# Optimization experiments

Measured on AMD Instinct MI355X. Metric: run time of the kernel, lower is better.

## Reference

```python
import jax, jax.numpy as jnp
import numpy as np

N = 100000          # nodes
C = 25000           # clusters in coding tree
E = 1000000         # edges
D = 64              # num_features == hidden_dim
NUM_BLOCKS = 2
N_CONVS = 2 * NUM_BLOCKS + 1
BN_EPS = 1e-5


def setup_inputs() -> dict:
    key = jax.random.key(0)
    ks = jax.random.split(key, 8)
    sc = 1.0 / np.sqrt(D)
    x = jax.random.normal(ks[0], (N, D), jnp.float32)
    edge_index = jax.random.randint(ks[1], (2, E), 0, N, dtype=jnp.int32)
    s_cluster = jax.random.randint(ks[2], (N,), 0, C, dtype=jnp.int32)
    conv_w = jax.random.normal(ks[3], (N_CONVS, D, D), jnp.float32) * sc
    conv_b = jnp.zeros((N_CONVS, D), jnp.float32)
    pool_w = jax.random.normal(ks[4], (2, D, D), jnp.float32) * sc
    pool_b = jnp.zeros((2, D), jnp.float32)
    bn_gamma = jnp.ones((2, D), jnp.float32)
    bn_beta = jnp.zeros((2, D), jnp.float32)
    return {"x": x, "edge_index": edge_index, "s_cluster": s_cluster,
            "conv_w": conv_w, "conv_b": conv_b, "pool_w": pool_w,
            "pool_b": pool_b, "bn_gamma": bn_gamma, "bn_beta": bn_beta}


def _gcn_norm(edge_index):
    # GCNConv default: add self-loops, symmetric normalization D^-1/2 (A+I) D^-1/2
    loop = jnp.arange(N, dtype=edge_index.dtype)
    row = jnp.concatenate([edge_index[0], loop])  # source nodes
    col = jnp.concatenate([edge_index[1], loop])  # target nodes
    deg = jax.ops.segment_sum(jnp.ones(row.shape[0], jnp.float32), col, num_segments=N)
    dinv = jnp.where(deg > 0, jax.lax.rsqrt(deg), 0.0)
    return row, col, dinv[row] * dinv[col]  # per-edge norm coefficient


def _gcn_conv(x, w, b, row, col, norm):
    h = x @ w                                     # [N, D] transform first (PyG GCNConv)
    msg = h[row] * norm[:, None]                  # gather + scale, [E+N, D]
    return jax.ops.segment_sum(msg, col, num_segments=N) + b


def _sepool(x, src_idx, dst_idx, out_size, w, b, gamma, beta):
    # SEPooling: scatter-add aggregation then nn = Linear -> ReLU -> BatchNorm1d
    agg = jax.ops.segment_sum(x[src_idx], dst_idx, num_segments=out_size)
    h = jax.nn.relu(agg @ w + b)
    mean = jnp.mean(h, axis=0)
    var = jnp.mean((h - mean) ** 2, axis=0)       # biased var, torch BN training mode
    return gamma * (h - mean) * jax.lax.rsqrt(var + BN_EPS) + beta


def reference(x, edge_index, s_cluster, conv_w, conv_b, pool_w, pool_b, bn_gamma, bn_beta):
    row, col, norm = _gcn_norm(edge_index)
    node_ids = jnp.arange(N, dtype=s_cluster.dtype)
    for i in range(NUM_BLOCKS):
        x = jax.nn.relu(_gcn_conv(x, conv_w[i], conv_b[i], row, col, norm))
    # pool down: nodes -> clusters (s_edge_index = [cluster, node], target_to_source)
    x = jax.nn.relu(_sepool(x, node_ids, s_cluster, C,
                            pool_w[0], pool_b[0], bn_gamma[0], bn_beta[0]))
    # pool up: clusters -> nodes (transposed assignment)
    x = jax.nn.relu(_sepool(x, s_cluster, node_ids, N,
                            pool_w[1], pool_b[1], bn_gamma[1], bn_beta[1]))
    for i in range(NUM_BLOCKS, 2 * NUM_BLOCKS):
        x = jax.nn.relu(_gcn_conv(x, conv_w[i], conv_b[i], row, col, norm))
    x = _gcn_conv(x, conv_w[N_CONVS - 1], conv_b[N_CONVS - 1], row, col, norm)
    return x
```

## Files before the change

kernel.cpp:

```cpp
#include <hip/hip_runtime.h>
#include <hip/hip_bf16.h>

#define NN 100000
#define CC 25000
#define EE 1000000
#define BN_EPS 1e-5f
#define NBINS 1563
#define BINCAP 1024
#define CHUNK 8192

typedef unsigned int u32;
typedef unsigned short u16;

__device__ __forceinline__ float lo2f(u32 p) { return __uint_as_float(p << 16); }
__device__ __forceinline__ float hi2f(u32 p) { return __uint_as_float(p & 0xFFFF0000u); }
__device__ __forceinline__ u16 f2bf(float f) {
    u32 u = __float_as_uint(f);
    u32 r = u + 0x7FFFu + ((u >> 16) & 1u);
    return (u16)(r >> 16);
}
__device__ __forceinline__ u32 pack2(float a, float b) {
    return (u32)f2bf(a) | ((u32)f2bf(b) << 16);
}

__global__ void fill_f_kernel(float* __restrict__ p, float v, int n) {
    int i = blockIdx.x * blockDim.x + threadIdx.x;
    if (i < n) p[i] = v;
}
__global__ void fill_i_kernel(int* __restrict__ p, int v, int n) {
    int i = blockIdx.x * blockDim.x + threadIdx.x;
    if (i < n) p[i] = v;
}
__global__ void init_bincur_kernel(int* __restrict__ p, int n) {
    int i = blockIdx.x * blockDim.x + threadIdx.x;
    if (i < n) p[i] = i * BINCAP;
}

__global__ void hist_kernel(const int* __restrict__ idx, int* __restrict__ deg, int n) {
    int e = blockIdx.x * blockDim.x + threadIdx.x;
    if (e < n) atomicAdd(&deg[idx[e]], 1);
}

__global__ __launch_bounds__(256) void bin_scatter_kernel(
    const int* __restrict__ row, const int* __restrict__ col,
    int* __restrict__ bincur, u32* __restrict__ edges, int E)
{
    __shared__ int cnt[NBINS];
    __shared__ int basep[NBINS];
    const int tid = threadIdx.x;
    const int e0 = blockIdx.x * CHUNK;
    const int e1 = min(e0 + CHUNK, E);
    for (int i = tid; i < NBINS; i += 256) cnt[i] = 0;
    __syncthreads();

    for (int i = e0 + tid; i < e1; i += 1024) {
        const int i1 = i + 256, i2 = i + 512, i3 = i + 768;
        int c0 = col[i];
        int c1 = (i1 < e1) ? col[i1] : 0;
        int c2 = (i2 < e1) ? col[i2] : 0;
        int c3 = (i3 < e1) ? col[i3] : 0;
        atomicAdd(&cnt[c0 >> 6], 1);
        if (i1 < e1) atomicAdd(&cnt[c1 >> 6], 1);
        if (i2 < e1) atomicAdd(&cnt[c2 >> 6], 1);
        if (i3 < e1) atomicAdd(&cnt[c3 >> 6], 1);
    }
    __syncthreads();

    for (int i = tid; i < NBINS; i += 256) {
        int c = cnt[i];
        if (c) basep[i] = atomicAdd(&bincur[i], c);
        cnt[i] = 0;
    }
    __syncthreads();

    for (int i = e0 + tid; i < e1; i += 1024) {
        const int i1 = i + 256, i2 = i + 512, i3 = i + 768;
        int c0 = col[i],                 r0 = row[i];
        int c1 = (i1 < e1) ? col[i1] : 0, r1 = (i1 < e1) ? row[i1] : 0;
        int c2 = (i2 < e1) ? col[i2] : 0, r2 = (i2 < e1) ? row[i2] : 0;
        int c3 = (i3 < e1) ? col[i3] : 0, r3 = (i3 < e1) ? row[i3] : 0;
        {
            int b = c0 >> 6;
            int p = basep[b] + atomicAdd(&cnt[b], 1);
            if (p < (b + 1) * BINCAP) edges[p] = (u32)r0 | ((u32)(c0 & 63) << 26);
        }
        if (i1 < e1) {
            int b = c1 >> 6;
            int p = basep[b] + atomicAdd(&cnt[b], 1);
            if (p < (b + 1) * BINCAP) edges[p] = (u32)r1 | ((u32)(c1 & 63) << 26);
        }
        if (i2 < e1) {
            int b = c2 >> 6;
            int p = basep[b] + atomicAdd(&cnt[b], 1);
            if (p < (b + 1) * BINCAP) edges[p] = (u32)r2 | ((u32)(c2 & 63) << 26);
        }
        if (i3 < e1) {
            int b = c3 >> 6;
            int p = basep[b] + atomicAdd(&cnt[b], 1);
            if (p < (b + 1) * BINCAP) edges[p] = (u32)r3 | ((u32)(c3 & 63) << 26);
        }
    }
}

__global__ __launch_bounds__(256) void deg_dinv_kernel(
    const int* __restrict__ bincur, const u32* __restrict__ edges,
    int* __restrict__ deg, float* __restrict__ dinv, int M)
{
    __shared__ int cnt[64];
    const int tid = threadIdx.x;
    if (tid < 64) cnt[tid] = 0;
    __syncthreads();
    const int eb = blockIdx.x * BINCAP;
    const int ee = bincur[blockIdx.x];
    for (int i = eb + tid; i < ee; i += 256)
        atomicAdd(&cnt[edges[i] >> 26], 1);
    __syncthreads();
    const int node = blockIdx.x * 64 + tid;
    if (tid < 64 && node < M) {
        deg[node] = cnt[tid];
        dinv[node] = rsqrtf((float)(cnt[tid] + 1));
    }
}

__global__ __launch_bounds__(256) void csr_scatter_kernel(
    const int* __restrict__ bincur, const u32* __restrict__ edges,
    const int* __restrict__ rowptr, int* __restrict__ csrc, int M)
{
    __shared__ int cur[64];
    const int tid = threadIdx.x;
    const int base = blockIdx.x * 64;
    if (tid < 64) cur[tid] = (base + tid < M) ? rowptr[base + tid] : 0;
    __syncthreads();
    const int eb = blockIdx.x * BINCAP;
    const int ee = bincur[blockIdx.x];
    for (int i = eb + tid; i < ee; i += 256) {
        u32 pk = edges[i];
        int slot = atomicAdd(&cur[pk >> 26], 1);
        csrc[slot] = (int)(pk & 0x03FFFFFFu);
    }
}

__global__ __launch_bounds__(256) void scan_block_kernel(const int* __restrict__ in,
                                                         int* __restrict__ out,
                                                         int* __restrict__ bsum, int n) {
    __shared__ int sh[256];
    const int tid = threadIdx.x;
    const int base = blockIdx.x * 1024 + tid * 4;
    int v0 = 0, v1 = 0, v2 = 0, v3 = 0;
    if (base + 0 < n) v0 = in[base + 0];
    if (base + 1 < n) v1 = in[base + 1];
    if (base + 2 < n) v2 = in[base + 2];
    if (base + 3 < n) v3 = in[base + 3];
    int s = v0 + v1 + v2 + v3;
    sh[tid] = s;
    __syncthreads();
    for (int off = 1; off < 256; off <<= 1) {
        int t = (tid >= off) ? sh[tid - off] : 0;
        __syncthreads();
        sh[tid] += t;
        __syncthreads();
    }
    int excl = sh[tid] - s;
    if (tid == 255) bsum[blockIdx.x] = sh[255];
    if (base + 0 < n) out[base + 0] = excl;
    if (base + 1 < n) out[base + 1] = excl + v0;
    if (base + 2 < n) out[base + 2] = excl + v0 + v1;
    if (base + 3 < n) out[base + 3] = excl + v0 + v1 + v2;
}

__global__ __launch_bounds__(256) void scan_top_kernel(int* __restrict__ bsum, int nb) {
    __shared__ int sh[256];
    const int tid = threadIdx.x;
    int v = (tid < nb) ? bsum[tid] : 0;
    sh[tid] = v;
    __syncthreads();
    for (int off = 1; off < 256; off <<= 1) {
        int t = (tid >= off) ? sh[tid - off] : 0;
        __syncthreads();
        sh[tid] += t;
        __syncthreads();
    }
    if (tid < nb) bsum[tid] = sh[tid] - v;
}

__global__ __launch_bounds__(256) void scan_add_kernel(int* __restrict__ p, int* __restrict__ cursor,
                                                       const int* __restrict__ bsum, int n, int total) {
    const int base = blockIdx.x * 1024;
    const int off = bsum[blockIdx.x];
    for (int j = threadIdx.x; j < 1024; j += 256) {
        int i = base + j;
        if (i < n) { int v = p[i] + off; p[i] = v; cursor[i] = v; }
    }
    if (blockIdx.x == 0 && threadIdx.x == 0) p[n] = total;
}

__global__ void scatter_iota_kernel(const int* __restrict__ cl,
                                    int* __restrict__ cursor, int* __restrict__ dst, int n) {
    int i = blockIdx.x * blockDim.x + threadIdx.x;
    if (i < n) { int p = atomicAdd(&cursor[cl[i]], 1); dst[p] = i; }
}

template <bool INF32, bool EDGEDINV>
__device__ __forceinline__ void acc_row(const void* __restrict__ Pv,
                                        const float* __restrict__ dinv, int r, int lc,
                                        float& s0, float& s1, float& s2, float& s3) {
    float d = EDGEDINV ? dinv[r] : 1.0f;
    if constexpr (INF32) {
        float4 v = ((const float4*)Pv)[(size_t)r * 16 + lc];
        if constexpr (EDGEDINV) {
            s0 = fmaf(v.x, d, s0); s1 = fmaf(v.y, d, s1);
            s2 = fmaf(v.z, d, s2); s3 = fmaf(v.w, d, s3);
        } else { s0 += v.x; s1 += v.y; s2 += v.z; s3 += v.w; }
    } else {
        uint2 p = ((const uint2*)Pv)[(size_t)r * 16 + lc];
        if constexpr (EDGEDINV) {
            s0 = fmaf(lo2f(p.x), d, s0); s1 = fmaf(hi2f(p.x), d, s1);
            s2 = fmaf(lo2f(p.y), d, s2); s3 = fmaf(hi2f(p.y), d, s3);
        } else { s0 += lo2f(p.x); s1 += hi2f(p.x); s2 += lo2f(p.y); s3 += hi2f(p.y); }
    }
}

template <int MODE, bool INF32, bool SCALEOUT, bool RELU, bool OUTF32>
__global__ __launch_bounds__(256, 8) void fused_mm_kernel(
    const int* __restrict__ rowptr, const int* __restrict__ src,
    const void* __restrict__ Pv, const float* __restrict__ W,
    const float* __restrict__ bias, const float* __restrict__ dinv,
    void* __restrict__ out, int M)
{
    __shared__ float Xs[64 * 68];

    const int tid = threadIdx.x;
    const int base = blockIdx.x * 64;

    {
        const int g = tid >> 4;
        const int lc = tid & 15;
        #pragma unroll
        for (int q = 0; q < 4; q++) {
            const int nl = g * 4 + q;
            const int node = base + nl;
            float s0 = 0.f, s1 = 0.f, s2 = 0.f, s3 = 0.f;
            if (node < M) {
                if constexpr (MODE == 2) {
                    acc_row<INF32, false>(Pv, dinv, src[node], lc, s0, s1, s2, s3);
                } else {
                    if constexpr (MODE == 0)
                        acc_row<INF32, true>(Pv, dinv, node, lc, s0, s1, s2, s3);
                    int i = rowptr[node];
                    const int pe = rowptr[node + 1];
                    for (; i + 4 <= pe; i += 4) {
                        int r0 = src[i], r1 = src[i + 1], r2 = src[i + 2], r3 = src[i + 3];
                        acc_row<INF32, MODE == 0>(Pv, dinv, r0, lc, s0, s1, s2, s3);
                        acc_row<INF32, MODE == 0>(Pv, dinv, r1, lc, s0, s1, s2, s3);
                        acc_row<INF32, MODE == 0>(Pv, dinv, r2, lc, s0, s1, s2, s3);
                        acc_row<INF32, MODE == 0>(Pv, dinv, r3, lc, s0, s1, s2, s3);
                    }
                    for (; i < pe; i++)
                        acc_row<INF32, MODE == 0>(Pv, dinv, src[i], lc, s0, s1, s2, s3);
                }
            }
            *(float4*)&Xs[nl * 68 + lc * 4] = make_float4(s0, s1, s2, s3);
        }
    }
    __syncthreads();

    const int c4 = tid & 15;
    const int rg = tid >> 4;
    const float* Wc = W + c4 * 4;

    float acc[4][4];
    #pragma unroll
    for (int r = 0; r < 4; r++)
        #pragma unroll
        for (int c = 0; c < 4; c++) acc[r][c] = 0.f;

    #pragma unroll 4
    for (int k0 = 0; k0 < 64; k0 += 4) {
        float4 w0 = *(const float4*)&Wc[(k0 + 0) * 64];
        float4 w1 = *(const float4*)&Wc[(k0 + 1) * 64];
        float4 w2 = *(const float4*)&Wc[(k0 + 2) * 64];
        float4 w3 = *(const float4*)&Wc[(k0 + 3) * 64];
        #pragma unroll
        for (int r = 0; r < 4; r++) {
            float4 xv = *(const float4*)&Xs[(rg * 4 + r) * 68 + k0];
            acc[r][0] = fmaf(xv.x, w0.x, acc[r][0]);
            acc[r][1] = fmaf(xv.x, w0.y, acc[r][1]);
            acc[r][2] = fmaf(xv.x, w0.z, acc[r][2]);
            acc[r][3] = fmaf(xv.x, w0.w, acc[r][3]);
            acc[r][0] = fmaf(xv.y, w1.x, acc[r][0]);
            acc[r][1] = fmaf(xv.y, w1.y, acc[r][1]);
            acc[r][2] = fmaf(xv.y, w1.z, acc[r][2]);
            acc[r][3] = fmaf(xv.y, w1.w, acc[r][3]);
            acc[r][0] = fmaf(xv.z, w2.x, acc[r][0]);
            acc[r][1] = fmaf(xv.z, w2.y, acc[r][1]);
            acc[r][2] = fmaf(xv.z, w2.z, acc[r][2]);
            acc[r][3] = fmaf(xv.z, w2.w, acc[r][3]);
            acc[r][0] = fmaf(xv.w, w3.x, acc[r][0]);
            acc[r][1] = fmaf(xv.w, w3.y, acc[r][1]);
            acc[r][2] = fmaf(xv.w, w3.z, acc[r][2]);
            acc[r][3] = fmaf(xv.w, w3.w, acc[r][3]);
        }
    }

    const float4 bv = *(const float4*)&bias[c4 * 4];
    #pragma unroll
    for (int r = 0; r < 4; r++) {
        int gr = base + rg * 4 + r;
        if (gr < M) {
            float v0 = acc[r][0], v1 = acc[r][1], v2 = acc[r][2], v3 = acc[r][3];
            if constexpr (SCALEOUT) {
                float d = dinv[gr];
                v0 *= d; v1 *= d; v2 *= d; v3 *= d;
            }
            v0 += bv.x; v1 += bv.y; v2 += bv.z; v3 += bv.w;
            if constexpr (RELU) {
                v0 = fmaxf(v0, 0.f); v1 = fmaxf(v1, 0.f);
                v2 = fmaxf(v2, 0.f); v3 = fmaxf(v3, 0.f);
            }
            if constexpr (OUTF32)
                ((float4*)out)[(size_t)gr * 16 + c4] = make_float4(v0, v1, v2, v3);
            else
                ((uint2*)out)[(size_t)gr * 16 + c4] = make_uint2(pack2(v0, v1), pack2(v2, v3));
        }
    }
}

__global__ __launch_bounds__(256) void bn_stats_kernel(const u32* __restrict__ H,
                                                       float* __restrict__ stats, int M)
{
    const int tid = threadIdx.x;
    const int c2 = tid & 31;
    const int rg = tid >> 5;
    float a0 = 0.f, a1 = 0.f, b0 = 0.f, b1 = 0.f;
    for (int r = blockIdx.x * 8 + rg; r < M; r += gridDim.x * 8) {
        u32 p = H[(size_t)r * 32 + c2];
        float x0 = lo2f(p), x1 = hi2f(p);
        a0 += x0; a1 += x1; b0 += x0 * x0; b1 += x1 * x1;
    }
    __shared__ float s0[256], s1[256], q0[256], q1[256];
    s0[tid] = a0; s1[tid] = a1; q0[tid] = b0; q1[tid] = b1;
    __syncthreads();
    if (tid < 64) {
        int cc2 = tid >> 1, sub = tid & 1;
        const float* sa = sub ? s1 : s0;
        const float* qa = sub ? q1 : q0;
        float a = 0.f, b = 0.f;
        #pragma unroll
        for (int g8 = 0; g8 < 8; g8++) { a += sa[g8 * 32 + cc2]; b += qa[g8 * 32 + cc2]; }
        atomicAdd(&stats[tid], a);
        atomicAdd(&stats[64 + tid], b);
    }
}

__global__ void bn_apply_kernel(const u32* __restrict__ H, u32* __restrict__ Y,
                                const float* __restrict__ stats,
                                const float* __restrict__ gamma, const float* __restrict__ beta,
                                int total32, float invM)
{
    int i = blockIdx.x * blockDim.x + threadIdx.x;
    if (i < total32) {
        int c2 = i & 31;
        float m0 = stats[c2 * 2] * invM,     m1 = stats[c2 * 2 + 1] * invM;
        float v0 = stats[64 + c2 * 2] * invM - m0 * m0;
        float v1 = stats[64 + c2 * 2 + 1] * invM - m1 * m1;
        u32 p = H[i];
        float x0 = gamma[c2 * 2]     * (lo2f(p) - m0) * rsqrtf(v0 + BN_EPS) + beta[c2 * 2];
        float x1 = gamma[c2 * 2 + 1] * (hi2f(p) - m1) * rsqrtf(v1 + BN_EPS) + beta[c2 * 2 + 1];
        Y[i] = pack2(fmaxf(x0, 0.f), fmaxf(x1, 0.f));
    }
}

extern "C" void kernel_launch(void* const* d_in, const int* in_sizes, int n_in,
                              void* d_out, int out_size, void* d_ws, size_t ws_size,
                              hipStream_t stream)
{
    const float* x     = (const float*)d_in[0];
    const int*   ei    = (const int*)  d_in[1];
    const int*   scl   = (const int*)  d_in[2];
    const float* cw    = (const float*)d_in[3];
    const float* cb    = (const float*)d_in[4];
    const float* pw    = (const float*)d_in[5];
    const float* pb    = (const float*)d_in[6];
    const float* gamma = (const float*)d_in[7];
    const float* beta  = (const float*)d_in[8];
    float* out = (float*)d_out;

    const int N = NN, C = CC, E = EE;
    const int* row = ei;
    const int* col = ei + E;

    char* w = (char*)d_ws;
    u16* A        = (u16*)w;              w += (size_t)N * 64 * 2;
    u16* B        = (u16*)w;              w += (size_t)N * 64 * 2;
    u16* cb0      = (u16*)w;              w += (size_t)C * 64 * 2;
    u16* cb1      = (u16*)w;              w += (size_t)C * 64 * 2;
    float* dinv   = (float*)w;            w += (size_t)N * 4;
    float* stats  = (float*)w;            w += 128 * 4;
    int* deg_i    = (int*)w;              w += (size_t)N * 4;
    int* rowptr   = (int*)w;              w += (size_t)(N + 4) * 4;
    int* cursor   = (int*)w;              w += (size_t)N * 4;
    int* csrc     = (int*)w;              w += (size_t)E * 4;
    u32* edges    = (u32*)w;              w += (size_t)NBINS * BINCAP * 4;
    int* bincur   = (int*)w;              w += (size_t)NBINS * 4;
    int* cdeg     = (int*)w;              w += (size_t)C * 4;
    int* crowptr  = (int*)w;              w += (size_t)(C + 4) * 4;
    int* ccursor  = (int*)w;              w += (size_t)C * 4;
    int* cnsrc    = (int*)w;              w += (size_t)N * 4;
    int* bsum     = (int*)w;              w += 256 * 4;

    const int TB = 256;
    dim3 blk(TB);
    const int NB_N = (N + 1023) / 1024;
    const int NB_C = (C + 1023) / 1024;
    const int NCHUNK = (E + CHUNK - 1) / CHUNK;
    const int GN = NBINS;
    const int GC = (C + 63) / 64;

    init_bincur_kernel<<<(NBINS + TB - 1) / TB, blk, 0, stream>>>(bincur, NBINS);
    bin_scatter_kernel<<<NCHUNK, blk, 0, stream>>>(row, col, bincur, edges, E);
    deg_dinv_kernel<<<NBINS, blk, 0, stream>>>(bincur, edges, deg_i, dinv, N);

    scan_block_kernel<<<NB_N, blk, 0, stream>>>(deg_i, rowptr, bsum, N);
    scan_top_kernel<<<1, blk, 0, stream>>>(bsum, NB_N);
    scan_add_kernel<<<NB_N, blk, 0, stream>>>(rowptr, cursor, bsum, N, E);
    csr_scatter_kernel<<<NBINS, blk, 0, stream>>>(bincur, edges, rowptr, csrc, N);

    fill_i_kernel<<<(C + TB - 1) / TB, blk, 0, stream>>>(cdeg, 0, C);
    hist_kernel<<<(N + TB - 1) / TB, blk, 0, stream>>>(scl, cdeg, N);
    scan_block_kernel<<<NB_C, blk, 0, stream>>>(cdeg, crowptr, bsum, C);
    scan_top_kernel<<<1, blk, 0, stream>>>(bsum, NB_C);
    scan_add_kernel<<<NB_C, blk, 0, stream>>>(crowptr, ccursor, bsum, C, N);
    scatter_iota_kernel<<<(N + TB - 1) / TB, blk, 0, stream>>>(scl, ccursor, cnsrc, N);

    fused_mm_kernel<0, true, true, true, false>
        <<<GN, blk, 0, stream>>>(rowptr, csrc, x, cw + 0 * 4096, cb + 0 * 64, dinv, A, N);
    fused_mm_kernel<0, false, true, true, false>
        <<<GN, blk, 0, stream>>>(rowptr, csrc, A, cw + 1 * 4096, cb + 1 * 64, dinv, B, N);

    fused_mm_kernel<1, false, false, true, false>
        <<<GC, blk, 0, stream>>>(crowptr, cnsrc, B, pw, pb, nullptr, cb1, C);
    fill_f_kernel<<<1, 128, 0, stream>>>(stats, 0.f, 128);
    bn_stats_kernel<<<512, blk, 0, stream>>>((const u32*)cb1, stats, C);
    bn_apply_kernel<<<(C * 32 + TB - 1) / TB, blk, 0, stream>>>(
        (const u32*)cb1, (u32*)cb0, stats, gamma, beta, C * 32, 1.0f / C);

    fused_mm_kernel<2, false, false, true, false>
        <<<GN, blk, 0, stream>>>(nullptr, scl, cb0, pw + 4096, pb + 64, nullptr, A, N);
    fill_f_kernel<<<1, 128, 0, stream>>>(stats, 0.f, 128);
    bn_stats_kernel<<<512, blk, 0, stream>>>((const u32*)A, stats, N);
    bn_apply_kernel<<<(N * 32 + TB - 1) / TB, blk, 0, stream>>>(
        (const u32*)A, (u32*)B, stats, gamma + 64, beta + 64, N * 32, 1.0f / N);

    fused_mm_kernel<0, false, true, true, false>
        <<<GN, blk, 0, stream>>>(rowptr, csrc, B, cw + 2 * 4096, cb + 2 * 64, dinv, A, N);
    fused_mm_kernel<0, false, true, true, false>
        <<<GN, blk, 0, stream>>>(rowptr, csrc, A, cw + 3 * 4096, cb + 3 * 64, dinv, B, N);
    fused_mm_kernel<0, false, true, false, true>
        <<<GN, blk, 0, stream>>>(rowptr, csrc, B, cw + 4 * 4096, cb + 4 * 64, dinv, out, N);
}
```

Before: 385.8 us.

## Pack source dinv with CSR indices and widen gather to 16-byte row loads

The CSR scatter now stores each edge's source index together with that source's dinv as an int2. The aggregation no longer needs a dependent random load of dinv[src] per edge. The gather phase also switches from 16 lanes × 8 bytes to 8 lanes × 16 bytes per row, with each thread handling 2 nodes instead of 4. This makes the bf16 row loads wider and gives each node more lanes. In exchange the edge metadata array doubles in size, and each thread holds 8 accumulators.

After: 388.0 us. About the same (+0.6%).

```diff
diff --git a/kernel.cpp b/kernel.cpp
--- a/kernel.cpp
+++ b/kernel.cpp
@@ -21,6 +21,25 @@
 }
 __device__ __forceinline__ u32 pack2(float a, float b) {
     return (u32)f2bf(a) | ((u32)f2bf(b) << 16);
+}
+
+__device__ __forceinline__ void accb(uint4 p, float d, float* s) {
+    s[0] = fmaf(lo2f(p.x), d, s[0]); s[1] = fmaf(hi2f(p.x), d, s[1]);
+    s[2] = fmaf(lo2f(p.y), d, s[2]); s[3] = fmaf(hi2f(p.y), d, s[3]);
+    s[4] = fmaf(lo2f(p.z), d, s[4]); s[5] = fmaf(hi2f(p.z), d, s[5]);
+    s[6] = fmaf(lo2f(p.w), d, s[6]); s[7] = fmaf(hi2f(p.w), d, s[7]);
+}
+__device__ __forceinline__ void accb_ns(uint4 p, float* s) {
+    s[0] += lo2f(p.x); s[1] += hi2f(p.x);
+    s[2] += lo2f(p.y); s[3] += hi2f(p.y);
+    s[4] += lo2f(p.z); s[5] += hi2f(p.z);
+    s[6] += lo2f(p.w); s[7] += hi2f(p.w);
+}
+__device__ __forceinline__ void accf(float4 a, float4 b, float d, float* s) {
+    s[0] = fmaf(a.x, d, s[0]); s[1] = fmaf(a.y, d, s[1]);
+    s[2] = fmaf(a.z, d, s[2]); s[3] = fmaf(a.w, d, s[3]);
+    s[4] = fmaf(b.x, d, s[4]); s[5] = fmaf(b.y, d, s[5]);
+    s[6] = fmaf(b.z, d, s[6]); s[7] = fmaf(b.w, d, s[7]);
 }
 
 __global__ void fill_f_kernel(float* __restrict__ p, float v, int n) {
@@ -124,7 +143,8 @@
 
 __global__ __launch_bounds__(256) void csr_scatter_kernel(
     const int* __restrict__ bincur, const u32* __restrict__ edges,
-    const int* __restrict__ rowptr, int* __restrict__ csrc, int M)
+    const int* __restrict__ rowptr, const float* __restrict__ dinv,
+    int2* __restrict__ csrc2, int M)
 {
     __shared__ int cur[64];
     const int tid = threadIdx.x;
@@ -135,8 +155,9 @@
     const int ee = bincur[blockIdx.x];
     for (int i = eb + tid; i < ee; i += 256) {
         u32 pk = edges[i];
+        int srcid = (int)(pk & 0x03FFFFFFu);
         int slot = atomicAdd(&cur[pk >> 26], 1);
-        csrc[slot] = (int)(pk & 0x03FFFFFFu);
+        csrc2[slot] = make_int2(srcid, __float_as_int(dinv[srcid]));
     }
 }
 
@@ -200,29 +221,9 @@
     if (i < n) { int p = atomicAdd(&cursor[cl[i]], 1); dst[p] = i; }
 }
 
-template <bool INF32, bool EDGEDINV>
-__device__ __forceinline__ void acc_row(const void* __restrict__ Pv,
-                                        const float* __restrict__ dinv, int r, int lc,
-                                        float& s0, float& s1, float& s2, float& s3) {
-    float d = EDGEDINV ? dinv[r] : 1.0f;
-    if constexpr (INF32) {
-        float4 v = ((const float4*)Pv)[(size_t)r * 16 + lc];
-        if constexpr (EDGEDINV) {
-            s0 = fmaf(v.x, d, s0); s1 = fmaf(v.y, d, s1);
-            s2 = fmaf(v.z, d, s2); s3 = fmaf(v.w, d, s3);
-        } else { s0 += v.x; s1 += v.y; s2 += v.z; s3 += v.w; }
-    } else {
-        uint2 p = ((const uint2*)Pv)[(size_t)r * 16 + lc];
-        if constexpr (EDGEDINV) {
-            s0 = fmaf(lo2f(p.x), d, s0); s1 = fmaf(hi2f(p.x), d, s1);
-            s2 = fmaf(lo2f(p.y), d, s2); s3 = fmaf(hi2f(p.y), d, s3);
-        } else { s0 += lo2f(p.x); s1 += hi2f(p.x); s2 += lo2f(p.y); s3 += hi2f(p.y); }
-    }
-}
-
 template <int MODE, bool INF32, bool SCALEOUT, bool RELU, bool OUTF32>
 __global__ __launch_bounds__(256, 8) void fused_mm_kernel(
-    const int* __restrict__ rowptr, const int* __restrict__ src,
+    const int* __restrict__ rowptr, const void* __restrict__ meta,
     const void* __restrict__ Pv, const float* __restrict__ W,
     const float* __restrict__ bias, const float* __restrict__ dinv,
     void* __restrict__ out, int M)
@@ -231,35 +232,85 @@
 
     const int tid = threadIdx.x;
     const int base = blockIdx.x * 64;
+    const uint4*  P8 = (const uint4*)Pv;
+    const float4* PF = (const float4*)Pv;
 
     {
-        const int g = tid >> 4;
-        const int lc = tid & 15;
+        const int g = tid >> 3;
+        const int lc = tid & 7;
         #pragma unroll
-        for (int q = 0; q < 4; q++) {
-            const int nl = g * 4 + q;
+        for (int q = 0; q < 2; q++) {
+            const int nl = g * 2 + q;
             const int node = base + nl;
-            float s0 = 0.f, s1 = 0.f, s2 = 0.f, s3 = 0.f;
+            float s[8];
+            #pragma unroll
+            for (int k = 0; k < 8; k++) s[k] = 0.f;
             if (node < M) {
                 if constexpr (MODE == 2) {
-                    acc_row<INF32, false>(Pv, dinv, src[node], lc, s0, s1, s2, s3);
+                    int r = ((const int*)meta)[node];
+                    accb_ns(P8[(size_t)r * 8 + lc], s);
+                } else if constexpr (MODE == 0) {
+                    {
+                        float d = dinv[node];
+                        if constexpr (INF32)
+                            accf(PF[(size_t)node * 16 + lc * 2],
+                                 PF[(size_t)node * 16 + lc * 2 + 1], d, s);
+                        else
+                            accb(P8[(size_t)node * 8 + lc], d, s);
+                    }
+                    const int2* m2 = (const int2*)meta;
+                    int i = rowptr[node];
+                    const int pe = rowptr[node + 1];
+                    if constexpr (!INF32) {
+                        for (; i + 4 <= pe; i += 4) {
+                            int2 ma = m2[i], mb = m2[i + 1], mc = m2[i + 2], md = m2[i + 3];
+                            uint4 p0 = P8[(size_t)ma.x * 8 + lc];
+                            uint4 p1 = P8[(size_t)mb.x * 8 + lc];
+                            uint4 p2 = P8[(size_t)mc.x * 8 + lc];
+                            uint4 p3 = P8[(size_t)md.x * 8 + lc];
+                            accb(p0, __int_as_float(ma.y), s);
+                            accb(p1, __int_as_float(mb.y), s);
+                            accb(p2, __int_as_float(mc.y), s);
+                            accb(p3, __int_as_float(md.y), s);
+                        }
+                        for (; i < pe; i++) {
+                            int2 ma = m2[i];
+                            accb(P8[(size_t)ma.x * 8 + lc], __int_as_float(ma.y), s);
+                        }
+                    } else {
+                        for (; i + 2 <= pe; i += 2) {
+                            int2 ma = m2[i], mb = m2[i + 1];
+                            float4 a0 = PF[(size_t)ma.x * 16 + lc * 2];
+                            float4 b0 = PF[(size_t)ma.x * 16 + lc * 2 + 1];
+                            float4 a1 = PF[(size_t)mb.x * 16 + lc * 2];
+                            float4 b1 = PF[(size_t)mb.x * 16 + lc * 2 + 1];
+                            accf(a0, b0, __int_as_float(ma.y), s);
+                            accf(a1, b1, __int_as_float(mb.y), s);
+                        }
+                        for (; i < pe; i++) {
+                            int2 ma = m2[i];
+                            accf(PF[(size_t)ma.x * 16 + lc * 2],
+                                 PF[(size_t)ma.x * 16 + lc * 2 + 1],
+                                 __int_as_float(ma.y), s);
+                        }
+                    }
                 } else {
-                    if constexpr (MODE == 0)
-                        acc_row<INF32, true>(Pv, dinv, node, lc, s0, s1, s2, s3);
+                    const int* m1a = (const int*)meta;
                     int i = rowptr[node];
                     const int pe = rowptr[node + 1];
                     for (; i + 4 <= pe; i += 4) {
-                        int r0 = src[i], r1 = src[i + 1], r2 = src[i + 2], r3 = src[i + 3];
-                        acc_row<INF32, MODE == 0>(Pv, dinv, r0, lc, s0, s1, s2, s3);
-                        acc_row<INF32, MODE == 0>(Pv, dinv, r1, lc, s0, s1, s2, s3);
-                        acc_row<INF32, MODE == 0>(Pv, dinv, r2, lc, s0, s1, s2, s3);
-                        acc_row<INF32, MODE == 0>(Pv, dinv, r3, lc, s0, s1, s2, s3);
+                        int r0 = m1a[i], r1 = m1a[i + 1], r2 = m1a[i + 2], r3 = m1a[i + 3];
+                        uint4 p0 = P8[(size_t)r0 * 8 + lc];
+                        uint4 p1 = P8[(size_t)r1 * 8 + lc];
+                        uint4 p2 = P8[(size_t)r2 * 8 + lc];
+                        uint4 p3 = P8[(size_t)r3 * 8 + lc];
+                        accb_ns(p0, s); accb_ns(p1, s); accb_ns(p2, s); accb_ns(p3, s);
                     }
-                    for (; i < pe; i++)
-                        acc_row<INF32, MODE == 0>(Pv, dinv, src[i], lc, s0, s1, s2, s3);
+                    for (; i < pe; i++) accb_ns(P8[(size_t)m1a[i] * 8 + lc], s);
                 }
             }
-            *(float4*)&Xs[nl * 68 + lc * 4] = make_float4(s0, s1, s2, s3);
+            *(float4*)&Xs[nl * 68 + lc * 8]     = make_float4(s[0], s[1], s[2], s[3]);
+            *(float4*)&Xs[nl * 68 + lc * 8 + 4] = make_float4(s[4], s[5], s[6], s[7]);
         }
     }
     __syncthreads();
@@ -399,7 +450,7 @@
     int* deg_i    = (int*)w;              w += (size_t)N * 4;
     int* rowptr   = (int*)w;              w += (size_t)(N + 4) * 4;
     int* cursor   = (int*)w;              w += (size_t)N * 4;
-    int* csrc     = (int*)w;              w += (size_t)E * 4;
+    int2* csrc2   = (int2*)w;             w += (size_t)E * 8;
     u32* edges    = (u32*)w;              w += (size_t)NBINS * BINCAP * 4;
     int* bincur   = (int*)w;              w += (size_t)NBINS * 4;
     int* cdeg     = (int*)w;              w += (size_t)C * 4;
@@ -423,7 +474,7 @@
     scan_block_kernel<<<NB_N, blk, 0, stream>>>(deg_i, rowptr, bsum, N);
     scan_top_kernel<<<1, blk, 0, stream>>>(bsum, NB_N);
     scan_add_kernel<<<NB_N, blk, 0, stream>>>(rowptr, cursor, bsum, N, E);
-    csr_scatter_kernel<<<NBINS, blk, 0, stream>>>(bincur, edges, rowptr, csrc, N);
+    csr_scatter_kernel<<<NBINS, blk, 0, stream>>>(bincur, edges, rowptr, dinv, csrc2, N);
 
     fill_i_kernel<<<(C + TB - 1) / TB, blk, 0, stream>>>(cdeg, 0, C);
     hist_kernel<<<(N + TB - 1) / TB, blk, 0, stream>>>(scl, cdeg, N);
@@ -433,9 +484,9 @@
     scatter_iota_kernel<<<(N + TB - 1) / TB, blk, 0, stream>>>(scl, ccursor, cnsrc, N);
 
     fused_mm_kernel<0, true, true, true, false>
-        <<<GN, blk, 0, stream>>>(rowptr, csrc, x, cw + 0 * 4096, cb + 0 * 64, dinv, A, N);
+        <<<GN, blk, 0, stream>>>(rowptr, csrc2, x, cw + 0 * 4096, cb + 0 * 64, dinv, A, N);
     fused_mm_kernel<0, false, true, true, false>
-        <<<GN, blk, 0, stream>>>(rowptr, csrc, A, cw + 1 * 4096, cb + 1 * 64, dinv, B, N);
+        <<<GN, blk, 0, stream>>>(rowptr, csrc2, A, cw + 1 * 4096, cb + 1 * 64, dinv, B, N);
 
     fused_mm_kernel<1, false, false, true, false>
         <<<GC, blk, 0, stream>>>(crowptr, cnsrc, B, pw, pb, nullptr, cb1, C);
@@ -452,9 +503,9 @@
         (const u32*)A, (u32*)B, stats, gamma + 64, beta + 64, N * 32, 1.0f / N);
 
     fused_mm_kernel<0, false, true, true, false>
-        <<<GN, blk, 0, stream>>>(rowptr, csrc, B, cw + 2 * 4096, cb + 2 * 64, dinv, A, N);
+        <<<GN, blk, 0, stream>>>(rowptr, csrc2, B, cw + 2 * 4096, cb + 2 * 64, dinv, A, N);
     fused_mm_kernel<0, false, true, true, false>
-        <<<GN, blk, 0, stream>>>(rowptr, csrc, A, cw + 3 * 4096, cb + 3 * 64, dinv, B, N);
+        <<<GN, blk, 0, stream>>>(rowptr, csrc2, A, cw + 3 * 4096, cb + 3 * 64, dinv, B, N);
     fused_mm_kernel<0, false, true, false, true>
-        <<<GN, blk, 0, stream>>>(rowptr, csrc, B, cw + 4 * 4096, cb + 4 * 64, dinv, out, N);
-}
+        <<<GN, blk, 0, stream>>>(rowptr, csrc2, B, cw + 4 * 4096, cb + 4 * 64, dinv, out, N);
+}
```

## Fold BatchNorm apply and ReLU into consumer gather kernels

Applied to the files above, without the earlier changes.

Removes the two standalone BatchNorm-apply passes and instead computes the per-channel affine scale and shift from the stats inside the next fused gather/matmul kernel, applying affine plus ReLU on every gathered row. The three small fill/init kernels are also merged into one launch, and the bin end index is clamped to the bin capacity. This drops a full read and write of the cluster and node feature arrays plus several launches. In exchange, the affine work is repeated per edge in the following GCN conv, about ten times more arithmetic than applying it once per node.

New measurement: 368.8 us, median of 2. 1.05x faster.

```diff
diff --git a/kernel.cpp b/kernel.cpp
--- a/kernel.cpp
+++ b/kernel.cpp
@@ -8,6 +8,7 @@
 #define NBINS 1563
 #define BINCAP 1024
 #define CHUNK 8192
+#define SRCMASK 0x03FFFFFFu
 
 typedef unsigned int u32;
 typedef unsigned short u16;
@@ -23,17 +24,12 @@
     return (u32)f2bf(a) | ((u32)f2bf(b) << 16);
 }
 
-__global__ void fill_f_kernel(float* __restrict__ p, float v, int n) {
+__global__ void init_misc_kernel(int* __restrict__ bincur, int* __restrict__ cdeg,
+                                 float* __restrict__ stats) {
     int i = blockIdx.x * blockDim.x + threadIdx.x;
-    if (i < n) p[i] = v;
-}
-__global__ void fill_i_kernel(int* __restrict__ p, int v, int n) {
-    int i = blockIdx.x * blockDim.x + threadIdx.x;
-    if (i < n) p[i] = v;
-}
-__global__ void init_bincur_kernel(int* __restrict__ p, int n) {
-    int i = blockIdx.x * blockDim.x + threadIdx.x;
-    if (i < n) p[i] = i * BINCAP;
+    if (i < NBINS) bincur[i] = i * BINCAP;
+    if (i < CC) cdeg[i] = 0;
+    if (i < 256) stats[i] = 0.f;
 }
 
 __global__ void hist_kernel(const int* __restrict__ idx, int* __restrict__ deg, int n) {
@@ -111,7 +107,7 @@
     if (tid < 64) cnt[tid] = 0;
     __syncthreads();
     const int eb = blockIdx.x * BINCAP;
-    const int ee = bincur[blockIdx.x];
+    const int ee = min(bincur[blockIdx.x], eb + BINCAP);
     for (int i = eb + tid; i < ee; i += 256)
         atomicAdd(&cnt[edges[i] >> 26], 1);
     __syncthreads();
@@ -132,11 +128,11 @@
     if (tid < 64) cur[tid] = (base + tid < M) ? rowptr[base + tid] : 0;
     __syncthreads();
     const int eb = blockIdx.x * BINCAP;
-    const int ee = bincur[blockIdx.x];
+    const int ee = min(bincur[blockIdx.x], eb + BINCAP);
     for (int i = eb + tid; i < ee; i += 256) {
         u32 pk = edges[i];
         int slot = atomicAdd(&cur[pk >> 26], 1);
-        csrc[slot] = (int)(pk & 0x03FFFFFFu);
+        csrc[slot] = (int)(pk & SRCMASK);
     }
 }
 
@@ -200,31 +196,39 @@
     if (i < n) { int p = atomicAdd(&cursor[cl[i]], 1); dst[p] = i; }
 }
 
-template <bool INF32, bool EDGEDINV>
+template <bool INF32, bool EDGEDINV, bool AFFINE>
 __device__ __forceinline__ void acc_row(const void* __restrict__ Pv,
                                         const float* __restrict__ dinv, int r, int lc,
+                                        const float* av, const float* bv,
                                         float& s0, float& s1, float& s2, float& s3) {
     float d = EDGEDINV ? dinv[r] : 1.0f;
+    float v0, v1, v2, v3;
     if constexpr (INF32) {
         float4 v = ((const float4*)Pv)[(size_t)r * 16 + lc];
-        if constexpr (EDGEDINV) {
-            s0 = fmaf(v.x, d, s0); s1 = fmaf(v.y, d, s1);
-            s2 = fmaf(v.z, d, s2); s3 = fmaf(v.w, d, s3);
-        } else { s0 += v.x; s1 += v.y; s2 += v.z; s3 += v.w; }
+        v0 = v.x; v1 = v.y; v2 = v.z; v3 = v.w;
     } else {
         uint2 p = ((const uint2*)Pv)[(size_t)r * 16 + lc];
-        if constexpr (EDGEDINV) {
-            s0 = fmaf(lo2f(p.x), d, s0); s1 = fmaf(hi2f(p.x), d, s1);
-            s2 = fmaf(lo2f(p.y), d, s2); s3 = fmaf(hi2f(p.y), d, s3);
-        } else { s0 += lo2f(p.x); s1 += hi2f(p.x); s2 += lo2f(p.y); s3 += hi2f(p.y); }
-    }
-}
-
-template <int MODE, bool INF32, bool SCALEOUT, bool RELU, bool OUTF32>
+        v0 = lo2f(p.x); v1 = hi2f(p.x); v2 = lo2f(p.y); v3 = hi2f(p.y);
+    }
+    if constexpr (AFFINE) {
+        v0 = fmaxf(fmaf(av[0], v0, bv[0]), 0.f);
+        v1 = fmaxf(fmaf(av[1], v1, bv[1]), 0.f);
+        v2 = fmaxf(fmaf(av[2], v2, bv[2]), 0.f);
+        v3 = fmaxf(fmaf(av[3], v3, bv[3]), 0.f);
+    }
+    if constexpr (EDGEDINV) {
+        s0 = fmaf(v0, d, s0); s1 = fmaf(v1, d, s1);
+        s2 = fmaf(v2, d, s2); s3 = fmaf(v3, d, s3);
+    } else { s0 += v0; s1 += v1; s2 += v2; s3 += v3; }
+}
+
+template <int MODE, bool INF32, bool AFFINE, bool SCALEOUT, bool RELU, bool OUTF32>
 __global__ __launch_bounds__(256, 8) void fused_mm_kernel(
     const int* __restrict__ rowptr, const int* __restrict__ src,
     const void* __restrict__ Pv, const float* __restrict__ W,
     const float* __restrict__ bias, const float* __restrict__ dinv,
+    const float* __restrict__ bst, const float* __restrict__ bng,
+    const float* __restrict__ bnb, float invM,
     void* __restrict__ out, int M)
 {
     __shared__ float Xs[64 * 68];
@@ -235,6 +239,21 @@
     {
         const int g = tid >> 4;
         const int lc = tid & 15;
+
+        float av[4] = {0.f, 0.f, 0.f, 0.f};
+        float bvv[4] = {0.f, 0.f, 0.f, 0.f};
+        if constexpr (AFFINE) {
+            #pragma unroll
+            for (int j = 0; j < 4; j++) {
+                int c = lc * 4 + j;
+                float m = bst[c] * invM;
+                float var = bst[64 + c] * invM - m * m;
+                float rs = rsqrtf(var + BN_EPS);
+                av[j] = bng[c] * rs;
+                bvv[j] = bnb[c] - m * av[j];
+            }
+        }
+
         #pragma unroll
         for (int q = 0; q < 4; q++) {
             const int nl = g * 4 + q;
@@ -242,21 +261,21 @@
             float s0 = 0.f, s1 = 0.f, s2 = 0.f, s3 = 0.f;
             if (node < M) {
                 if constexpr (MODE == 2) {
-                    acc_row<INF32, false>(Pv, dinv, src[node], lc, s0, s1, s2, s3);
+                    acc_row<INF32, false, AFFINE>(Pv, dinv, src[node], lc, av, bvv, s0, s1, s2, s3);
                 } else {
                     if constexpr (MODE == 0)
-                        acc_row<INF32, true>(Pv, dinv, node, lc, s0, s1, s2, s3);
+                        acc_row<INF32, true, AFFINE>(Pv, dinv, node, lc, av, bvv, s0, s1, s2, s3);
                     int i = rowptr[node];
                     const int pe = rowptr[node + 1];
                     for (; i + 4 <= pe; i += 4) {
                         int r0 = src[i], r1 = src[i + 1], r2 = src[i + 2], r3 = src[i + 3];
-                        acc_row<INF32, MODE == 0>(Pv, dinv, r0, lc, s0, s1, s2, s3);
-                        acc_row<INF32, MODE == 0>(Pv, dinv, r1, lc, s0, s1, s2, s3);
-                        acc_row<INF32, MODE == 0>(Pv, dinv, r2, lc, s0, s1, s2, s3);
-                        acc_row<INF32, MODE == 0>(Pv, dinv, r3, lc, s0, s1, s2, s3);
+                        acc_row<INF32, MODE == 0, AFFINE>(Pv, dinv, r0, lc, av, bvv, s0, s1, s2, s3);
+                        acc_row<INF32, MODE == 0, AFFINE>(Pv, dinv, r1, lc, av, bvv, s0, s1, s2, s3);
+                        acc_row<INF32, MODE == 0, AFFINE>(Pv, dinv, r2, lc, av, bvv, s0, s1, s2, s3);
+                        acc_row<INF32, MODE == 0, AFFINE>(Pv, dinv, r3, lc, av, bvv, s0, s1, s2, s3);
                     }
                     for (; i < pe; i++)
-                        acc_row<INF32, MODE == 0>(Pv, dinv, src[i], lc, s0, s1, s2, s3);
+                        acc_row<INF32, MODE == 0, AFFINE>(Pv, dinv, src[i], lc, av, bvv, s0, s1, s2, s3);
                 }
             }
             *(float4*)&Xs[nl * 68 + lc * 4] = make_float4(s0, s1, s2, s3);
@@ -352,24 +371,6 @@
     }
 }
 
-__global__ void bn_apply_kernel(const u32* __restrict__ H, u32* __restrict__ Y,
-                                const float* __restrict__ stats,
-                                const float* __restrict__ gamma, const float* __restrict__ beta,
-                                int total32, float invM)
-{
-    int i = blockIdx.x * blockDim.x + threadIdx.x;
-    if (i < total32) {
-        int c2 = i & 31;
-        float m0 = stats[c2 * 2] * invM,     m1 = stats[c2 * 2 + 1] * invM;
-        float v0 = stats[64 + c2 * 2] * invM - m0 * m0;
-        float v1 = stats[64 + c2 * 2 + 1] * invM - m1 * m1;
-        u32 p = H[i];
-        float x0 = gamma[c2 * 2]     * (lo2f(p) - m0) * rsqrtf(v0 + BN_EPS) + beta[c2 * 2];
-        float x1 = gamma[c2 * 2 + 1] * (hi2f(p) - m1) * rsqrtf(v1 + BN_EPS) + beta[c2 * 2 + 1];
-        Y[i] = pack2(fmaxf(x0, 0.f), fmaxf(x1, 0.f));
-    }
-}
-
 extern "C" void kernel_launch(void* const* d_in, const int* in_sizes, int n_in,
                               void* d_out, int out_size, void* d_ws, size_t ws_size,
                               hipStream_t stream)
@@ -392,10 +393,9 @@
     char* w = (char*)d_ws;
     u16* A        = (u16*)w;              w += (size_t)N * 64 * 2;
     u16* B        = (u16*)w;              w += (size_t)N * 64 * 2;
-    u16* cb0      = (u16*)w;              w += (size_t)C * 64 * 2;
     u16* cb1      = (u16*)w;              w += (size_t)C * 64 * 2;
     float* dinv   = (float*)w;            w += (size_t)N * 4;
-    float* stats  = (float*)w;            w += 128 * 4;
+    float* stats  = (float*)w;            w += 256 * 4;
     int* deg_i    = (int*)w;              w += (size_t)N * 4;
     int* rowptr   = (int*)w;              w += (size_t)(N + 4) * 4;
     int* cursor   = (int*)w;              w += (size_t)N * 4;
@@ -408,6 +408,9 @@
     int* cnsrc    = (int*)w;              w += (size_t)N * 4;
     int* bsum     = (int*)w;              w += 256 * 4;
 
+    float* stats0 = stats;
+    float* stats1 = stats + 128;
+
     const int TB = 256;
     dim3 blk(TB);
     const int NB_N = (N + 1023) / 1024;
@@ -416,7 +419,7 @@
     const int GN = NBINS;
     const int GC = (C + 63) / 64;
 
-    init_bincur_kernel<<<(NBINS + TB - 1) / TB, blk, 0, stream>>>(bincur, NBINS);
+    init_misc_kernel<<<(C + TB - 1) / TB, blk, 0, stream>>>(bincur, cdeg, stats);
     bin_scatter_kernel<<<NCHUNK, blk, 0, stream>>>(row, col, bincur, edges, E);
     deg_dinv_kernel<<<NBINS, blk, 0, stream>>>(bincur, edges, deg_i, dinv, N);
 
@@ -425,36 +428,36 @@
     scan_add_kernel<<<NB_N, blk, 0, stream>>>(rowptr, cursor, bsum, N, E);
     csr_scatter_kernel<<<NBINS, blk, 0, stream>>>(bincur, edges, rowptr, csrc, N);
 
-    fill_i_kernel<<<(C + TB - 1) / TB, blk, 0, stream>>>(cdeg, 0, C);
     hist_kernel<<<(N + TB - 1) / TB, blk, 0, stream>>>(scl, cdeg, N);
     scan_block_kernel<<<NB_C, blk, 0, stream>>>(cdeg, crowptr, bsum, C);
     scan_top_kernel<<<1, blk, 0, stream>>>(bsum, NB_C);
     scan_add_kernel<<<NB_C, blk, 0, stream>>>(crowptr, ccursor, bsum, C, N);
     scatter_iota_kernel<<<(N + TB - 1) / TB, blk, 0, stream>>>(scl, ccursor, cnsrc, N);
 
-    fused_mm_kernel<0, true, true, true, false>
-        <<<GN, blk, 0, stream>>>(rowptr, csrc, x, cw + 0 * 4096, cb + 0 * 64, dinv, A, N);
-    fused_mm_kernel<0, false, true, true, false>
-        <<<GN, blk, 0, stream>>>(rowptr, csrc, A, cw + 1 * 4096, cb + 1 * 64, dinv, B, N);
-
-    fused_mm_kernel<1, false, false, true, false>
-        <<<GC, blk, 0, stream>>>(crowptr, cnsrc, B, pw, pb, nullptr, cb1, C);
-    fill_f_kernel<<<1, 128, 0, stream>>>(stats, 0.f, 128);
-    bn_stats_kernel<<<512, blk, 0, stream>>>((const u32*)cb1, stats, C);
-    bn_apply_kernel<<<(C * 32 + TB - 1) / TB, blk, 0, stream>>>(
-        (const u32*)cb1, (u32*)cb0, stats, gamma, beta, C * 32, 1.0f / C);
-
-    fused_mm_kernel<2, false, false, true, false>
-        <<<GN, blk, 0, stream>>>(nullptr, scl, cb0, pw + 4096, pb + 64, nullptr, A, N);
-    fill_f_kernel<<<1, 128, 0, stream>>>(stats, 0.f, 128);
-    bn_stats_kernel<<<512, blk, 0, stream>>>((const u32*)A, stats, N);
-    bn_apply_kernel<<<(N * 32 + TB - 1) / TB, blk, 0, stream>>>(
-        (const u32*)A, (u32*)B, stats, gamma + 64, beta + 64, N * 32, 1.0f / N);
-
-    fused_mm_kernel<0, false, true, true, false>
-        <<<GN, blk, 0, stream>>>(rowptr, csrc, B, cw + 2 * 4096, cb + 2 * 64, dinv, A, N);
-    fused_mm_kernel<0, false, true, true, false>
-        <<<GN, blk, 0, stream>>>(rowptr, csrc, A, cw + 3 * 4096, cb + 3 * 64, dinv, B, N);
-    fused_mm_kernel<0, false, true, false, true>
-        <<<GN, blk, 0, stream>>>(rowptr, csrc, B, cw + 4 * 4096, cb + 4 * 64, dinv, out, N);
-}
+    fused_mm_kernel<0, true, false, true, true, false>
+        <<<GN, blk, 0, stream>>>(rowptr, csrc, x, cw + 0 * 4096, cb + 0 * 64, dinv,
+                                 nullptr, nullptr, nullptr, 0.f, A, N);
+    fused_mm_kernel<0, false, false, true, true, false>
+        <<<GN, blk, 0, stream>>>(rowptr, csrc, A, cw + 1 * 4096, cb + 1 * 64, dinv,
+                                 nullptr, nullptr, nullptr, 0.f, B, N);
+
+    fused_mm_kernel<1, false, false, false, true, false>
+        <<<GC, blk, 0, stream>>>(crowptr, cnsrc, B, pw, pb, nullptr,
+                                 nullptr, nullptr, nullptr, 0.f, cb1, C);
+    bn_stats_kernel<<<512, blk, 0, stream>>>((const u32*)cb1, stats0, C);
+
+    fused_mm_kernel<2, false, true, false, true, false>
+        <<<GN, blk, 0, stream>>>(nullptr, scl, cb1, pw + 4096, pb + 64, nullptr,
+                                 stats0, gamma, beta, 1.0f / C, A, N);
+    bn_stats_kernel<<<512, blk, 0, stream>>>((const u32*)A, stats1, N);
+
+    fused_mm_kernel<0, false, true, true, true, false>
+        <<<GN, blk, 0, stream>>>(rowptr, csrc, A, cw + 2 * 4096, cb + 2 * 64, dinv,
+                                 stats1, gamma + 64, beta + 64, 1.0f / N, B, N);
+    fused_mm_kernel<0, false, false, true, true, false>
+        <<<GN, blk, 0, stream>>>(rowptr, csrc, B, cw + 3 * 4096, cb + 3 * 64, dinv,
+                                 nullptr, nullptr, nullptr, 0.f, A, N);
+    fused_mm_kernel<0, false, false, true, false, true>
+        <<<GN, blk, 0, stream>>>(rowptr, csrc, A, cw + 4 * 4096, cb + 4 * 64, dinv,
+                                 nullptr, nullptr, nullptr, 0.f, out, N);
+}
```
